# Kernel tuning notes

Hardware: AMD Instinct MI355X
Metric: run time of the kernel (lower is better)

The kernel has to match this reference:

```python
import jax, jax.numpy as jnp
import numpy as np

# scNET (vae_flag=False, cd=False, eval mode): genes x cells matrix;
# PPI graph over 3000 genes, KNN graph over 4096 cells.
N_GENES, N_CELLS = 3000, 4096          # col_dim, row_dim
INTER_R, EMBD_R = 512, 128             # gene (rows) encoder dims
INTER_C, EMBD_C = 1024, 256            # cell (cols) encoder dims
N_LAYERS = 2
KNN_E, PPI_E = 65536, 262144
SCALE_PARAM = 3.0                      # TransformerConvReducrLayer scale_param


def setup_inputs() -> dict:
    key = jax.random.key(0)
    ks = iter(jax.random.split(key, 64))
    def lin(shape):
        fan_in = shape[-2]
        return jax.random.normal(next(ks), shape, jnp.float32) / np.sqrt(fan_in)
    inp = {}
    inp["x"] = jax.random.normal(next(ks), (N_GENES, N_CELLS), jnp.float32)
    inp["knn_ei"] = jax.random.randint(next(ks), (2, KNN_E), 0, N_CELLS)
    inp["ppi_ei"] = jax.random.randint(next(ks), (2, PPI_E), 0, N_GENES)
    inp["rl_W"] = lin((N_CELLS, N_CELLS)); inp["rl_b"] = jnp.zeros((N_CELLS,), jnp.float32)
    inp["rs_Wl"] = lin((N_LAYERS, N_CELLS, N_CELLS)); inp["rs_Wr"] = lin((N_LAYERS, N_CELLS, N_CELLS))
    inp["rs_b"] = jnp.zeros((N_LAYERS, N_CELLS), jnp.float32)
    inp["cs_Wl"] = lin((N_LAYERS, N_GENES, N_GENES)); inp["cs_Wr"] = lin((N_LAYERS, N_GENES, N_GENES))
    inp["cs_b"] = jnp.zeros((N_LAYERS, N_GENES), jnp.float32)
    inp["rg_W"] = lin((N_CELLS, INTER_R)); inp["rg_b"] = jnp.zeros((INTER_R,), jnp.float32)
    for nm in ("rq", "rk", "rv", "rsk"):
        inp[nm + "_W"] = lin((INTER_R, EMBD_R)); inp[nm + "_b"] = jnp.zeros((EMBD_R,), jnp.float32)
    inp["cg_W"] = lin((N_GENES, INTER_C)); inp["cg_b"] = jnp.zeros((INTER_C,), jnp.float32)
    for nm in ("cq", "ck", "cv", "csk"):
        inp[nm + "_W"] = lin((INTER_C, EMBD_C)); inp[nm + "_b"] = jnp.zeros((EMBD_C,), jnp.float32)
    inp["d1_W"] = lin((EMBD_C, INTER_C)); inp["d1_b"] = jnp.zeros((INTER_C,), jnp.float32)
    inp["d2_W"] = lin((INTER_C, INTER_C)); inp["d2_b"] = jnp.zeros((INTER_C,), jnp.float32)
    inp["d3_W"] = lin((INTER_C, N_GENES)); inp["d3_b"] = jnp.zeros((N_GENES,), jnp.float32)
    return inp


def sage_conv(x, ei, Wl, Wr, b):
    # PyG SAGEConv (mean aggr, root weight): lin_l(mean_{j->i} x_j) + lin_r(x_i) + b
    n = x.shape[0]
    src, dst = ei[0], ei[1]
    s = jax.ops.segment_sum(x[src], dst, num_segments=n)
    cnt = jax.ops.segment_sum(jnp.ones((ei.shape[1],), x.dtype), dst, num_segments=n)
    agg = s / jnp.maximum(cnt, 1.0)[:, None]
    return agg @ Wl + x @ Wr + b


def gcn_conv(x, ei, W, b):
    # PyG GCNConv: self loops + symmetric D^-1/2 (A+I) D^-1/2 normalization
    n = x.shape[0]
    idx = jnp.arange(n)
    src = jnp.concatenate([ei[0], idx])
    dst = jnp.concatenate([ei[1], idx])
    deg = jax.ops.segment_sum(jnp.ones((src.shape[0],), x.dtype), dst, num_segments=n)
    dinv = jax.lax.rsqrt(jnp.maximum(deg, 1.0))
    h = x @ W
    msg = h[src] * (dinv[src] * dinv[dst])[:, None]
    return jax.ops.segment_sum(msg, dst, num_segments=n) + b


def transformer_conv(x, ei, Wq, bq, Wk, bk, Wv, bv, Ws, bs, scale_param):
    # PyG TransformerConv (heads=1). scale_param=None -> per-destination segment
    # softmax; otherwise scNET's globally sigmoid-normalized attention
    # (TransformerConvReducrLayer.message): global mean/std standardize -> sigmoid.
    n = x.shape[0]
    d = Wq.shape[1]
    src, dst = ei[0], ei[1]
    q = x @ Wq + bq
    k = x @ Wk + bk
    v = x @ Wv + bv
    alpha = (q[dst] * k[src]).sum(-1) / jnp.sqrt(jnp.asarray(d, x.dtype))  # [E]
    if scale_param is None:
        m = jax.ops.segment_max(alpha, dst, num_segments=n)
        e = jnp.exp(alpha - m[dst])
        z = jax.ops.segment_sum(e, dst, num_segments=n)
        alpha = e / (z[dst] + 1e-16)
    else:
        alpha = (alpha - alpha.mean()) / ((1.0 / scale_param) * jnp.std(alpha, ddof=1))
        alpha = jax.nn.sigmoid(alpha)
    out = jax.ops.segment_sum(v[src] * alpha[:, None], dst, num_segments=n)
    return out + (x @ Ws + bs)  # root skip (lin_skip)


def reference(x, knn_ei, ppi_ei, rl_W, rl_b, rs_Wl, rs_Wr, rs_b, cs_Wl, cs_Wr, cs_b,
              rg_W, rg_b, rq_W, rq_b, rk_W, rk_b, rv_W, rv_b, rsk_W, rsk_b,
              cg_W, cg_b, cq_W, cq_b, ck_W, ck_b, cv_W, cv_b, csk_W, csk_b,
              d1_W, d1_b, d2_W, d2_b, d3_W, d3_b):
    # MutaelEncoder: row linear then alternating col/row SAGE layers (dropout=id in eval)
    h = x @ rl_W + rl_b                                   # [G, C]
    for i in range(N_LAYERS):
        h = jax.nn.leaky_relu(sage_conv(h.T, knn_ei, cs_Wl[i], cs_Wr[i], cs_b[i]), 0.01).T
        h = jax.nn.leaky_relu(sage_conv(h, ppi_ei, rs_Wl[i], rs_Wr[i], rs_b[i]), 0.01)
    # rows (gene) DimEncoder: GCN -> LeakyReLU -> TransformerConv (softmax attention)
    r = jax.nn.leaky_relu(gcn_conv(h, ppi_ei, rg_W, rg_b), 0.01)
    row_embed = transformer_conv(r, ppi_ei, rq_W, rq_b, rk_W, rk_b, rv_W, rv_b, rsk_W, rsk_b, None)
    # cols (cell) DimEncoder (reducer): GCN -> LeakyReLU -> sigmoid-normalized attention
    c = jax.nn.leaky_relu(gcn_conv(h.T, knn_ei, cg_W, cg_b), 0.01)
    col_embed = transformer_conv(c, knn_ei, cq_W, cq_b, ck_W, ck_b, cv_W, cv_b, csk_W, csk_b, SCALE_PARAM)
    # FatureDecoder (cd=False): 3-layer MLP with ReLU (dropout=id in eval)
    d = jax.nn.relu(col_embed @ d1_W + d1_b)
    d = jax.nn.relu(d @ d2_W + d2_b)
    recon = d @ d3_W + d3_b                               # [C_cells, G]
    return row_embed, col_embed, recon
```

## Files before the change

### kernel.cpp

```cpp
#include <hip/hip_runtime.h>
#include <math.h>

#define N_GENES 3000
#define N_CELLS 4096
#define GPAD    3072
#define INTER_R 512
#define EMBD_R  128
#define INTER_C 1024
#define EMBD_C  256
#define KNN_E   65536
#define PPI_E   262144

typedef unsigned short u16;
typedef __bf16 bf16x8 __attribute__((ext_vector_type(8)));
typedef float f32x4 __attribute__((ext_vector_type(4)));

__device__ __forceinline__ float b2f(u16 u) {
  union { unsigned i; float f; } x; x.i = ((unsigned)u) << 16; return x.f;
}
__device__ __forceinline__ u16 f2b(float f) {
  union { float f; unsigned i; } x; x.f = f;
  unsigned r = (x.i + 0x7FFFu + ((x.i >> 16) & 1u)) >> 16;
  return (u16)r;
}

typedef const void __attribute__((address_space(1))) gvoid;
typedef void __attribute__((address_space(3))) svoid;
__device__ __forceinline__ void gload16(const void* g, void* l) {
  __builtin_amdgcn_global_load_lds((gvoid*)g, (svoid*)l, 16, 0, 0);
}

template <int OUTF32>
__global__ __launch_bounds__(256) void mgemm_k(
    const u16* __restrict__ A, int lda, const u16* __restrict__ BT, int ldb,
    const float* __restrict__ bias, void* __restrict__ Cv, int ldc,
    int M, int N, int K, int accum, int act, int nbx) {
  __shared__ u16 As[2][128 * 32];
  __shared__ u16 Bs[2][128 * 32];
  const int t = threadIdx.x;
  const int w = t >> 6, l = t & 63;
  const int wr = w >> 1, wc = w & 1;
  const int fr = l & 15, hi = l >> 4;

  int nwg = gridDim.x;
  int bid = blockIdx.x;
  int q = nwg >> 3, r = nwg & 7, xcd = bid & 7, seq = bid >> 3;
  int sid = (xcd < r ? xcd * (q + 1) : r * (q + 1) + (xcd - r) * q) + seq;
  int by = sid / nbx, bx = sid - by * nbx;
  const int row0 = by * 128, col0 = bx * 128;

  f32x4 acc[4][4];
#pragma unroll
  for (int i = 0; i < 4; i++)
#pragma unroll
    for (int j = 0; j < 4; j++) acc[i][j] = (f32x4){0.f, 0.f, 0.f, 0.f};

  const u16* Aad[2]; const u16* Bad[2];
  char* Alds[2]; char* Blds[2];
#pragma unroll
  for (int c = 0; c < 2; c++) {
    int P = (w * 2 + c) * 64 + l;
    int prow = P >> 2, pg = (P & 3) ^ (prow & 3);
    int ar = row0 + prow; ar = ar < M ? ar : M - 1;
    int br = col0 + prow; br = br < N ? br : N - 1;
    Aad[c] = A + (size_t)ar * lda + pg * 8;
    Bad[c] = BT + (size_t)br * ldb + pg * 8;
    Alds[c] = (char*)&As[0][0] + (w * 2 + c) * 1024;
    Blds[c] = (char*)&Bs[0][0] + (w * 2 + c) * 1024;
  }
  const int nt = K >> 5;
  auto stage = [&](int tt, int b) {
    int ko = tt << 5;
#pragma unroll
    for (int c = 0; c < 2; c++) {
      gload16(Aad[c] + ko, Alds[c] + b * 8192);
      gload16(Bad[c] + ko, Blds[c] + b * 8192);
    }
  };
  auto compute = [&](int tt) {
    const u16* Ab = As[tt & 1];
    const u16* Bb = Bs[tt & 1];
    bf16x8 af[4], bfr[4];
#pragma unroll
    for (int mi = 0; mi < 4; mi++) {
      int row = wr * 64 + mi * 16 + fr;
      af[mi] = *(const bf16x8*)&Ab[row * 32 + ((hi ^ (row & 3)) << 3)];
    }
#pragma unroll
    for (int ni = 0; ni < 4; ni++) {
      int row = wc * 64 + ni * 16 + fr;
      bfr[ni] = *(const bf16x8*)&Bb[row * 32 + ((hi ^ (row & 3)) << 3)];
    }
    __builtin_amdgcn_s_setprio(1);
#pragma unroll
    for (int mi = 0; mi < 4; mi++)
#pragma unroll
      for (int ni = 0; ni < 4; ni++)
        acc[mi][ni] = __builtin_amdgcn_mfma_f32_16x16x32_bf16(
            af[mi], bfr[ni], acc[mi][ni], 0, 0, 0);
    __builtin_amdgcn_s_setprio(0);
  };

  stage(0, 0);
  if (nt > 1) stage(1, 1);
  for (int tt = 0; tt < nt - 1; tt++) {
    asm volatile("s_waitcnt vmcnt(4)" ::: "memory");
    __builtin_amdgcn_sched_barrier(0);
    __builtin_amdgcn_s_barrier();
    __builtin_amdgcn_sched_barrier(0);
    compute(tt);
    __builtin_amdgcn_sched_barrier(0);
    __builtin_amdgcn_s_barrier();
    __builtin_amdgcn_sched_barrier(0);
    if (tt + 2 < nt) stage(tt + 2, tt & 1);
  }
  asm volatile("s_waitcnt vmcnt(0)" ::: "memory");
  __builtin_amdgcn_sched_barrier(0);
  __builtin_amdgcn_s_barrier();
  __builtin_amdgcn_sched_barrier(0);
  compute(nt - 1);

#pragma unroll
  for (int mi = 0; mi < 4; mi++) {
    int mb = row0 + wr * 64 + mi * 16 + hi * 4;
#pragma unroll
    for (int rr2 = 0; rr2 < 4; rr2++) {
      int m = mb + rr2;
      if (m >= M) continue;
#pragma unroll
      for (int ni = 0; ni < 4; ni++) {
        int n = col0 + wc * 64 + ni * 16 + fr;
        if (n >= N) continue;
        float v = acc[mi][ni][rr2];
        if (bias) v += bias[n];
        if (OUTF32) {
          float* C = (float*)Cv;
          if (accum) v += C[(size_t)m * ldc + n];
          if (act == 1) v = v > 0.f ? v : 0.01f * v;
          else if (act == 2) v = fmaxf(v, 0.f);
          C[(size_t)m * ldc + n] = v;
        } else {
          u16* C = (u16*)Cv;
          if (accum) v += b2f(C[(size_t)m * ldc + n]);
          if (act == 1) v = v > 0.f ? v : 0.01f * v;
          else if (act == 2) v = fmaxf(v, 0.f);
          C[(size_t)m * ldc + n] = f2b(v);
        }
      }
    }
  }
}

__global__ void cvtw_k(const float* __restrict__ in, int K, int Nw,
                       u16* __restrict__ out, int ldb, int Kpad) {
  __shared__ float tile[32][33];
  int k0 = blockIdx.y * 32, n0 = blockIdx.x * 32;
  int tx = threadIdx.x & 31, ty = threadIdx.x >> 5;
  for (int i = ty; i < 32; i += 8)
    tile[i][tx] = (k0 + i < K && n0 + tx < Nw) ? in[(size_t)(k0 + i) * Nw + n0 + tx] : 0.f;
  __syncthreads();
  for (int i = ty; i < 32; i += 8) {
    int n = n0 + i, k = k0 + tx;
    if (n < Nw && k < Kpad) out[(size_t)n * ldb + k] = f2b(tile[tx][i]);
  }
}

__global__ void tpad_k(const u16* __restrict__ in, int R, int C, int lin,
                       u16* __restrict__ out, int ldout) {
  __shared__ u16 tile[32][33];
  int r0 = blockIdx.y * 32, c0 = blockIdx.x * 32;
  int tx = threadIdx.x & 31, ty = threadIdx.x >> 5;
  for (int i = ty; i < 32; i += 8)
    tile[i][tx] = (r0 + i < R && c0 + tx < C) ? in[(size_t)(r0 + i) * lin + c0 + tx] : (u16)0;
  __syncthreads();
  for (int i = ty; i < 32; i += 8) {
    int c = c0 + i, r = r0 + tx;
    if (c < C && r < ldout) out[(size_t)c * ldout + r] = tile[tx][i];
  }
}

__global__ void cvtx_k(const float* __restrict__ in, u16* __restrict__ out, int n) {
  int i = (blockIdx.x * 256 + threadIdx.x) * 4;
  if (i >= n) return;
  float4 v = *(const float4*)&in[i];
  uint2 o;
  o.x = (unsigned)f2b(v.x) | ((unsigned)f2b(v.y) << 16);
  o.y = (unsigned)f2b(v.z) | ((unsigned)f2b(v.w) << 16);
  *(uint2*)&out[i] = o;
}

__global__ void catbias_k(const float* b0, const float* b1, const float* b2,
                          const float* b3, int seg, float* out) {
  int i = blockIdx.x * 256 + threadIdx.x;
  if (i >= 4 * seg) return;
  const float* s = i < seg ? b0 : i < 2 * seg ? b1 : i < 3 * seg ? b2 : b3;
  out[i] = s[i & (seg - 1)];
}

__global__ void zero_i32(int* __restrict__ p, int n) {
  int i = blockIdx.x * 256 + threadIdx.x;
  if (i < n) p[i] = 0;
}
__global__ void count_k(const int* __restrict__ dst, int E, int* __restrict__ cnt) {
  int e = blockIdx.x * 256 + threadIdx.x;
  if (e < E) atomicAdd(&cnt[dst[e]], 1);
}
__global__ __launch_bounds__(1024) void scan_k(const int* __restrict__ cnt,
                                               int* __restrict__ rs, int N) {
  __shared__ int sd[1024];
  int t = threadIdx.x;
  int per = (N + 1023) >> 10;
  int base = t * per;
  int loc[4];
  int s = 0;
  for (int u = 0; u < per; u++) {
    int idx = base + u;
    loc[u] = s;
    int v = (idx < N) ? cnt[idx] : 0;
    s += v;
  }
  sd[t] = s;
  __syncthreads();
  for (int off = 1; off < 1024; off <<= 1) {
    int v = (t >= off) ? sd[t - off] : 0;
    __syncthreads();
    sd[t] += v;
    __syncthreads();
  }
  int prev = (t > 0) ? sd[t - 1] : 0;
  for (int u = 0; u < per; u++) {
    int idx = base + u;
    if (idx < N) rs[idx] = prev + loc[u];
  }
  if (t == 0) rs[N] = sd[1023];
}
__global__ void fill_k(const int* __restrict__ src, const int* __restrict__ dst, int E,
                       const int* __restrict__ rs, int* cursor,
                       int* __restrict__ csrc, int* __restrict__ ceid) {
  int e = blockIdx.x * 256 + threadIdx.x;
  if (e >= E) return;
  int d = dst[e];
  int p = atomicAdd(&cursor[d], 1);
  int b = rs[d] + p;
  csrc[b] = src[e];
  ceid[b] = e;
}
__global__ void dinv_k(const int* __restrict__ rs, float* __restrict__ dinv, int N) {
  int i = blockIdx.x * 256 + threadIdx.x;
  if (i < N) dinv[i] = rsqrtf((float)(rs[i + 1] - rs[i] + 1));
}

__global__ void sage_agg_k(const u16* __restrict__ X, int ld, const int* __restrict__ rs,
                           const int* __restrict__ csrc, u16* __restrict__ out,
                           int D, int Dpad) {
  int i = blockIdx.y;
  int j8 = (blockIdx.x * 256 + threadIdx.x) * 8;
  if (j8 >= Dpad) return;
  uint4 zo = {0, 0, 0, 0};
  if (j8 >= D) { *(uint4*)&out[(size_t)i * ld + j8] = zo; return; }
  int s = rs[i], e = rs[i + 1];
  float a[8] = {0, 0, 0, 0, 0, 0, 0, 0};
  for (int p = s; p < e; p++) {
    uint4 v = *(const uint4*)&X[(size_t)csrc[p] * ld + j8];
    a[0] += b2f(v.x & 0xffff); a[1] += b2f(v.x >> 16);
    a[2] += b2f(v.y & 0xffff); a[3] += b2f(v.y >> 16);
    a[4] += b2f(v.z & 0xffff); a[5] += b2f(v.z >> 16);
    a[6] += b2f(v.w & 0xffff); a[7] += b2f(v.w >> 16);
  }
  float inv = 1.f / fmaxf((float)(e - s), 1.f);
  uint4 o;
  o.x = (unsigned)f2b(a[0] * inv) | ((unsigned)f2b(a[1] * inv) << 16);
  o.y = (unsigned)f2b(a[2] * inv) | ((unsigned)f2b(a[3] * inv) << 16);
  o.z = (unsigned)f2b(a[4] * inv) | ((unsigned)f2b(a[5] * inv) << 16);
  o.w = (unsigned)f2b(a[6] * inv) | ((unsigned)f2b(a[7] * inv) << 16);
  *(uint4*)&out[(size_t)i * ld + j8] = o;
}

__global__ void gcn_agg_k(const u16* __restrict__ HW, int ld, const int* __restrict__ rs,
                          const int* __restrict__ csrc, const float* __restrict__ dinv,
                          const float* __restrict__ bias, u16* __restrict__ out, int D) {
  int i = blockIdx.y;
  int j8 = (blockIdx.x * 256 + threadIdx.x) * 8;
  if (j8 >= D) return;
  int s = rs[i], e = rs[i + 1];
  float a[8] = {0, 0, 0, 0, 0, 0, 0, 0};
  for (int p = s; p < e; p++) {
    int sr = csrc[p];
    float w = dinv[sr];
    uint4 v = *(const uint4*)&HW[(size_t)sr * ld + j8];
    a[0] += b2f(v.x & 0xffff) * w; a[1] += b2f(v.x >> 16) * w;
    a[2] += b2f(v.y & 0xffff) * w; a[3] += b2f(v.y >> 16) * w;
    a[4] += b2f(v.z & 0xffff) * w; a[5] += b2f(v.z >> 16) * w;
    a[6] += b2f(v.w & 0xffff) * w; a[7] += b2f(v.w >> 16) * w;
  }
  float di = dinv[i];
  uint4 sv = *(const uint4*)&HW[(size_t)i * ld + j8];
  float sf[8] = {b2f(sv.x & 0xffff), b2f(sv.x >> 16), b2f(sv.y & 0xffff), b2f(sv.y >> 16),
                 b2f(sv.z & 0xffff), b2f(sv.z >> 16), b2f(sv.w & 0xffff), b2f(sv.w >> 16)};
  unsigned o[4];
#pragma unroll
  for (int q = 0; q < 4; q++) {
    float v0 = di * a[2 * q] + sf[2 * q] * di * di + bias[j8 + 2 * q];
    float v1 = di * a[2 * q + 1] + sf[2 * q + 1] * di * di + bias[j8 + 2 * q + 1];
    v0 = v0 > 0.f ? v0 : 0.01f * v0;
    v1 = v1 > 0.f ? v1 : 0.01f * v1;
    o[q] = (unsigned)f2b(v0) | ((unsigned)f2b(v1) << 16);
  }
  *(uint4*)&out[(size_t)i * ld + j8] = *(uint4*)o;
}

__global__ void attn_row_k(const u16* __restrict__ QKVS, const int* __restrict__ rs,
                           const int* __restrict__ csrc, float* __restrict__ out, int N) {
  int node = blockIdx.x * 4 + (threadIdx.x >> 6);
  if (node >= N) return;
  int lane = threadIdx.x & 63;
  const u16* base = QKVS + (size_t)node * 512;
  unsigned qb = *(const unsigned*)&base[lane * 2];
  float qx = b2f(qb & 0xffff), qy = b2f(qb >> 16);
  int s = rs[node], e = rs[node + 1];
  float m = -1e30f, z = 0.f, ax = 0.f, ay = 0.f;
  const float scale = 0.08838834764831845f;
  for (int p = s; p < e; p++) {
    const u16* kb = QKVS + (size_t)csrc[p] * 512;
    unsigned kw = *(const unsigned*)&kb[128 + lane * 2];
    float part = qx * b2f(kw & 0xffff) + qy * b2f(kw >> 16);
#pragma unroll
    for (int off = 32; off; off >>= 1) part += __shfl_xor(part, off);
    float a = part * scale;
    float mn = fmaxf(m, a);
    float sc = __expf(m - mn);
    float wv = __expf(a - mn);
    z = z * sc + wv;
    unsigned vw = *(const unsigned*)&kb[256 + lane * 2];
    ax = ax * sc + wv * b2f(vw & 0xffff);
    ay = ay * sc + wv * b2f(vw >> 16);
    m = mn;
  }
  float inv = (e == s) ? 0.f : 1.f / (z + 1e-16f);
  unsigned sw = *(const unsigned*)&base[384 + lane * 2];
  out[(size_t)node * 128 + lane * 2] = ax * inv + b2f(sw & 0xffff);
  out[(size_t)node * 128 + lane * 2 + 1] = ay * inv + b2f(sw >> 16);
}

__global__ void col_alpha_k(const u16* __restrict__ QKVS, const int* __restrict__ src,
                            const int* __restrict__ dst, float* __restrict__ alpha, int E) {
  int e = blockIdx.x * 4 + (threadIdx.x >> 6);
  if (e >= E) return;
  int lane = threadIdx.x & 63;
  uint2 qb = *(const uint2*)&QKVS[(size_t)dst[e] * 1024 + lane * 4];
  uint2 kb = *(const uint2*)&QKVS[(size_t)src[e] * 1024 + 256 + lane * 4];
  float p = b2f(qb.x & 0xffff) * b2f(kb.x & 0xffff) + b2f(qb.x >> 16) * b2f(kb.x >> 16) +
            b2f(qb.y & 0xffff) * b2f(kb.y & 0xffff) + b2f(qb.y >> 16) * b2f(kb.y >> 16);
#pragma unroll
  for (int off = 32; off; off >>= 1) p += __shfl_xor(p, off);
  if (lane == 0) alpha[e] = p * 0.0625f;
}

__global__ void stats_k(const float* __restrict__ alpha, int E, double* __restrict__ st) {
  __shared__ double s1[256], s2[256];
  int t = threadIdx.x;
  double a1 = 0, a2 = 0;
  for (int i = blockIdx.x * 256 + t; i < E; i += gridDim.x * 256) {
    double a = alpha[i];
    a1 += a; a2 += a * a;
  }
  s1[t] = a1; s2[t] = a2;
  __syncthreads();
  for (int off = 128; off; off >>= 1) {
    if (t < off) { s1[t] += s1[t + off]; s2[t] += s2[t + off]; }
    __syncthreads();
  }
  if (t == 0) { atomicAdd(&st[0], s1[0]); atomicAdd(&st[1], s2[0]); }
}

__global__ void col_attn_agg_k(const u16* __restrict__ QKVS, const float* __restrict__ alpha,
                               const int* __restrict__ rs, const int* __restrict__ csrc,
                               const int* __restrict__ ceid, const double* __restrict__ st,
                               float* __restrict__ outf, u16* __restrict__ outb, int E) {
  int i = blockIdx.x;
  int j = threadIdx.x;
  double mean = st[0] / E;
  double var = (st[1] - E * mean * mean) / (double)(E - 1);
  float rstd = (float)(1.0 / sqrt(var));
  float fm = (float)mean;
  int s = rs[i], e = rs[i + 1];
  float acc = 0.f;
  for (int p = s; p < e; p++) {
    float a = alpha[ceid[p]];
    float x = 3.0f * (a - fm) * rstd;
    float sg = 1.f / (1.f + __expf(-x));
    acc += sg * b2f(QKVS[(size_t)csrc[p] * 1024 + 512 + j]);
  }
  float res = acc + b2f(QKVS[(size_t)i * 1024 + 768 + j]);
  outf[(size_t)i * 256 + j] = res;
  outb[(size_t)i * 256 + j] = f2b(res);
}

extern "C" void kernel_launch(void* const* d_in, const int* in_sizes, int n_in,
                              void* d_out, int out_size, void* d_ws, size_t ws_size,
                              hipStream_t stream) {
  const float* x      = (const float*)d_in[0];
  const int*   knn_ei = (const int*)d_in[1];
  const int*   ppi_ei = (const int*)d_in[2];
  const float* rl_W   = (const float*)d_in[3];
  const float* rl_b   = (const float*)d_in[4];
  const float* rs_Wl  = (const float*)d_in[5];
  const float* rs_Wr  = (const float*)d_in[6];
  const float* rs_b   = (const float*)d_in[7];
  const float* cs_Wl  = (const float*)d_in[8];
  const float* cs_Wr  = (const float*)d_in[9];
  const float* cs_b   = (const float*)d_in[10];
  const float* rg_W   = (const float*)d_in[11];
  const float* rg_b   = (const float*)d_in[12];
  const float* rq_W   = (const float*)d_in[13];
  const float* rq_b   = (const float*)d_in[14];
  const float* rk_W   = (const float*)d_in[15];
  const float* rk_b   = (const float*)d_in[16];
  const float* rv_W   = (const float*)d_in[17];
  const float* rv_b   = (const float*)d_in[18];
  const float* rsk_W  = (const float*)d_in[19];
  const float* rsk_b  = (const float*)d_in[20];
  const float* cg_W   = (const float*)d_in[21];
  const float* cg_b   = (const float*)d_in[22];
  const float* cq_W   = (const float*)d_in[23];
  const float* cq_b   = (const float*)d_in[24];
  const float* ck_W   = (const float*)d_in[25];
  const float* ck_b   = (const float*)d_in[26];
  const float* cv_W   = (const float*)d_in[27];
  const float* cv_b   = (const float*)d_in[28];
  const float* csk_W  = (const float*)d_in[29];
  const float* csk_b  = (const float*)d_in[30];
  const float* d1_W   = (const float*)d_in[31];
  const float* d1_b   = (const float*)d_in[32];
  const float* d2_W   = (const float*)d_in[33];
  const float* d2_b   = (const float*)d_in[34];
  const float* d3_W   = (const float*)d_in[35];
  const float* d3_b   = (const float*)d_in[36];
  float* out = (float*)d_out;

  char* ws = (char*)d_ws;
  size_t off = 0;
  auto alloc = [&](size_t bytes) -> void* {
    void* p = ws + off;
    off = (off + bytes + 255) & ~(size_t)255;
    return p;
  };
  const size_t PB = (size_t)N_CELLS * GPAD * 2;
  u16* P0 = (u16*)alloc(PB);
  u16* P1 = (u16*)alloc(PB);
  u16* P2 = (u16*)alloc(PB);
  u16* P3 = (u16*)alloc(PB);
  u16* xb  = (u16*)alloc((size_t)N_GENES * N_CELLS * 2);
  u16* BTs = (u16*)alloc((size_t)N_CELLS * N_CELLS * 2);
  u16* CEb = (u16*)alloc((size_t)N_CELLS * EMBD_C * 2);
  float* catb = (float*)alloc(1024 * 4);
  int* knn_rs  = (int*)alloc((N_CELLS + 1) * 4);
  int* knn_cnt = (int*)alloc(N_CELLS * 4);
  int* knn_cur = (int*)alloc(N_CELLS * 4);
  int* knn_src = (int*)alloc(KNN_E * 4);
  int* knn_eid = (int*)alloc(KNN_E * 4);
  int* ppi_rs  = (int*)alloc((N_GENES + 1) * 4);
  int* ppi_cnt = (int*)alloc(N_GENES * 4);
  int* ppi_cur = (int*)alloc(N_GENES * 4);
  int* ppi_src = (int*)alloc(PPI_E * 4);
  int* ppi_eid = (int*)alloc(PPI_E * 4);
  float* dinv_knn = (float*)alloc(N_CELLS * 4);
  float* dinv_ppi = (float*)alloc(N_GENES * 4);
  float* alphaB   = (float*)alloc(KNN_E * 4);
  double* stats   = (double*)alloc(2 * 8);

  auto cvtw = [&](const float* W, int K, int Nw, u16* dst, int ldb, int Kpad) {
    dim3 g((Nw + 31) / 32, (Kpad + 31) / 32);
    cvtw_k<<<g, 256, 0, stream>>>(W, K, Nw, dst, ldb, Kpad);
  };
  auto mg = [&](const u16* A, int lda, const u16* BT, int ldb, const float* bias,
                void* C, int ldc, int M, int N, int K, int accum, int act, int outf32) {
    int nbx = (N + 127) / 128, nby = (M + 127) / 128;
    dim3 g(nbx * nby);
    if (outf32)
      mgemm_k<1><<<g, 256, 0, stream>>>(A, lda, BT, ldb, bias, C, ldc, M, N, K, accum, act, nbx);
    else
      mgemm_k<0><<<g, 256, 0, stream>>>(A, lda, BT, ldb, bias, C, ldc, M, N, K, accum, act, nbx);
  };
  auto tpad = [&](const u16* in, int R, int C, int lin, u16* o, int ldout) {
    dim3 g((C + 31) / 32, (ldout + 31) / 32);
    tpad_k<<<g, 256, 0, stream>>>(in, R, C, lin, o, ldout);
  };
  auto sage = [&](const u16* X, int ld, const int* rs, const int* csrc, u16* o,
                  int nodes, int D, int Dpad) {
    dim3 g((Dpad / 8 + 255) / 256, nodes);
    sage_agg_k<<<g, 256, 0, stream>>>(X, ld, rs, csrc, o, D, Dpad);
  };
  auto gcn = [&](const u16* HW, int ld, const int* rs, const int* csrc, const float* dinv,
                 const float* bias, u16* o, int nodes, int D) {
    dim3 g((D / 8 + 255) / 256, nodes);
    gcn_agg_k<<<g, 256, 0, stream>>>(HW, ld, rs, csrc, dinv, bias, o, D);
  };

  zero_i32<<<(N_CELLS + 255) / 256, 256, 0, stream>>>(knn_cnt, N_CELLS);
  count_k<<<(KNN_E + 255) / 256, 256, 0, stream>>>(knn_ei + KNN_E, KNN_E, knn_cnt);
  scan_k<<<1, 1024, 0, stream>>>(knn_cnt, knn_rs, N_CELLS);
  zero_i32<<<(N_CELLS + 255) / 256, 256, 0, stream>>>(knn_cur, N_CELLS);
  fill_k<<<(KNN_E + 255) / 256, 256, 0, stream>>>(knn_ei, knn_ei + KNN_E, KNN_E,
                                                  knn_rs, knn_cur, knn_src, knn_eid);
  dinv_k<<<(N_CELLS + 255) / 256, 256, 0, stream>>>(knn_rs, dinv_knn, N_CELLS);
  zero_i32<<<(N_GENES + 255) / 256, 256, 0, stream>>>(ppi_cnt, N_GENES);
  count_k<<<(PPI_E + 255) / 256, 256, 0, stream>>>(ppi_ei + PPI_E, PPI_E, ppi_cnt);
  scan_k<<<1, 1024, 0, stream>>>(ppi_cnt, ppi_rs, N_GENES);
  zero_i32<<<(N_GENES + 255) / 256, 256, 0, stream>>>(ppi_cur, N_GENES);
  fill_k<<<(PPI_E + 255) / 256, 256, 0, stream>>>(ppi_ei, ppi_ei + PPI_E, PPI_E,
                                                  ppi_rs, ppi_cur, ppi_src, ppi_eid);
  dinv_k<<<(N_GENES + 255) / 256, 256, 0, stream>>>(ppi_rs, dinv_ppi, N_GENES);

  cvtx_k<<<(N_GENES * N_CELLS / 4 + 255) / 256, 256, 0, stream>>>(
      x, xb, N_GENES * N_CELLS);
  cvtw(rl_W, N_CELLS, N_CELLS, BTs, N_CELLS, N_CELLS);
  mg(xb, N_CELLS, BTs, N_CELLS, rl_b, P0, N_CELLS, N_GENES, N_CELLS, N_CELLS, 0, 0, 0);

  for (int i = 0; i < 2; i++) {
    const float* cWl = cs_Wl + (size_t)i * N_GENES * N_GENES;
    const float* cWr = cs_Wr + (size_t)i * N_GENES * N_GENES;
    const float* cb  = cs_b + (size_t)i * N_GENES;
    const float* rWl = rs_Wl + (size_t)i * N_CELLS * N_CELLS;
    const float* rWr = rs_Wr + (size_t)i * N_CELLS * N_CELLS;
    const float* rb  = rs_b + (size_t)i * N_CELLS;
    tpad(P0, N_GENES, N_CELLS, N_CELLS, P1, GPAD);
    sage(P1, GPAD, knn_rs, knn_src, P2, N_CELLS, N_GENES, GPAD);
    cvtw(cWl, N_GENES, N_GENES, BTs, GPAD, GPAD);
    mg(P2, GPAD, BTs, GPAD, cb, P3, GPAD, N_CELLS, N_GENES, GPAD, 0, 0, 0);
    cvtw(cWr, N_GENES, N_GENES, BTs, GPAD, GPAD);
    mg(P1, GPAD, BTs, GPAD, nullptr, P3, GPAD, N_CELLS, N_GENES, GPAD, 1, 1, 0);
    tpad(P3, N_CELLS, N_GENES, GPAD, P2, N_CELLS);
    sage(P2, N_CELLS, ppi_rs, ppi_src, P1, N_GENES, N_CELLS, N_CELLS);
    cvtw(rWl, N_CELLS, N_CELLS, BTs, N_CELLS, N_CELLS);
    mg(P1, N_CELLS, BTs, N_CELLS, rb, P0, N_CELLS, N_GENES, N_CELLS, N_CELLS, 0, 0, 0);
    cvtw(rWr, N_CELLS, N_CELLS, BTs, N_CELLS, N_CELLS);
    mg(P2, N_CELLS, BTs, N_CELLS, nullptr, P0, N_CELLS, N_GENES, N_CELLS, N_CELLS, 1, 1, 0);
  }

  cvtw(rg_W, N_CELLS, INTER_R, BTs, N_CELLS, N_CELLS);
  mg(P0, N_CELLS, BTs, N_CELLS, nullptr, P1, INTER_R, N_GENES, INTER_R, N_CELLS, 0, 0, 0);
  gcn(P1, INTER_R, ppi_rs, ppi_src, dinv_ppi, rg_b, P2, N_GENES, INTER_R);
  cvtw(rq_W, INTER_R, EMBD_R, BTs + (size_t)0 * EMBD_R * INTER_R, INTER_R, INTER_R);
  cvtw(rk_W, INTER_R, EMBD_R, BTs + (size_t)1 * EMBD_R * INTER_R, INTER_R, INTER_R);
  cvtw(rv_W, INTER_R, EMBD_R, BTs + (size_t)2 * EMBD_R * INTER_R, INTER_R, INTER_R);
  cvtw(rsk_W, INTER_R, EMBD_R, BTs + (size_t)3 * EMBD_R * INTER_R, INTER_R, INTER_R);
  catbias_k<<<2, 256, 0, stream>>>(rq_b, rk_b, rv_b, rsk_b, EMBD_R, catb);
  mg(P2, INTER_R, BTs, INTER_R, catb, P1, 4 * EMBD_R, N_GENES, 4 * EMBD_R, INTER_R, 0, 0, 0);
  attn_row_k<<<(N_GENES + 3) / 4, 256, 0, stream>>>(P1, ppi_rs, ppi_src, out, N_GENES);

  tpad(P0, N_GENES, N_CELLS, N_CELLS, P1, GPAD);
  cvtw(cg_W, N_GENES, INTER_C, BTs, GPAD, GPAD);
  mg(P1, GPAD, BTs, GPAD, nullptr, P2, INTER_C, N_CELLS, INTER_C, GPAD, 0, 0, 0);
  gcn(P2, INTER_C, knn_rs, knn_src, dinv_knn, cg_b, P0, N_CELLS, INTER_C);
  cvtw(cq_W, INTER_C, EMBD_C, BTs + (size_t)0 * EMBD_C * INTER_C, INTER_C, INTER_C);
  cvtw(ck_W, INTER_C, EMBD_C, BTs + (size_t)1 * EMBD_C * INTER_C, INTER_C, INTER_C);
  cvtw(cv_W, INTER_C, EMBD_C, BTs + (size_t)2 * EMBD_C * INTER_C, INTER_C, INTER_C);
  cvtw(csk_W, INTER_C, EMBD_C, BTs + (size_t)3 * EMBD_C * INTER_C, INTER_C, INTER_C);
  catbias_k<<<4, 256, 0, stream>>>(cq_b, ck_b, cv_b, csk_b, EMBD_C, catb);
  mg(P0, INTER_C, BTs, INTER_C, catb, P1, 4 * EMBD_C, N_CELLS, 4 * EMBD_C, INTER_C, 0, 0, 0);
  col_alpha_k<<<KNN_E / 4, 256, 0, stream>>>(P1, knn_ei, knn_ei + KNN_E, alphaB, KNN_E);
  zero_i32<<<1, 256, 0, stream>>>((int*)stats, 4);
  stats_k<<<64, 256, 0, stream>>>(alphaB, KNN_E, stats);
  float* col_embed = out + (size_t)N_GENES * EMBD_R;
  col_attn_agg_k<<<N_CELLS, 256, 0, stream>>>(P1, alphaB, knn_rs, knn_src, knn_eid,
                                              stats, col_embed, CEb, KNN_E);

  float* recon = col_embed + (size_t)N_CELLS * EMBD_C;
  cvtw(d1_W, EMBD_C, INTER_C, BTs, EMBD_C, EMBD_C);
  mg(CEb, EMBD_C, BTs, EMBD_C, d1_b, P2, INTER_C, N_CELLS, INTER_C, EMBD_C, 0, 2, 0);
  cvtw(d2_W, INTER_C, INTER_C, BTs, INTER_C, INTER_C);
  mg(P2, INTER_C, BTs, INTER_C, d2_b, P3, INTER_C, N_CELLS, INTER_C, INTER_C, 0, 2, 0);
  cvtw(d3_W, INTER_C, N_GENES, BTs, INTER_C, INTER_C);
  mg(P3, INTER_C, BTs, INTER_C, d3_b, recon, N_GENES, N_CELLS, N_GENES, INTER_C, 0, 0, 1);
}
```

Baseline: 2.461 ms.

## Fuse SAGE lin_l and lin_r GEMMs via concatenated K and repack LDS tiles

Each SAGE layer's two GEMMs (aggregated features times Wl plus root features times Wr, with accumulate) become one GEMM with doubled K. The aggregated and root matrices sit side by side in one buffer, and the weights are concatenated along K. This removes a second pass that read and wrote the output and launched an extra kernel, and it drops the separate zero-padding writes. The GEMM's LDS layout also changes from 128x32 to 64x64 row pairs with a new swizzle, which could change bank conflicts. Buffers are re-aliased, which risks overlap mistakes.

```diff
diff --git a/kernel.cpp b/kernel.cpp
--- a/kernel.cpp
+++ b/kernel.cpp
@@ -35,15 +35,14 @@
     const u16* __restrict__ A, int lda, const u16* __restrict__ BT, int ldb,
     const float* __restrict__ bias, void* __restrict__ Cv, int ldc,
     int M, int N, int K, int accum, int act, int nbx) {
-  __shared__ u16 As[2][128 * 32];
-  __shared__ u16 Bs[2][128 * 32];
+  __shared__ u16 As[2][64 * 64];
+  __shared__ u16 Bs[2][64 * 64];
   const int t = threadIdx.x;
   const int w = t >> 6, l = t & 63;
   const int wr = w >> 1, wc = w & 1;
   const int fr = l & 15, hi = l >> 4;
 
-  int nwg = gridDim.x;
-  int bid = blockIdx.x;
+  int nwg = gridDim.x, bid = blockIdx.x;
   int q = nwg >> 3, r = nwg & 7, xcd = bid & 7, seq = bid >> 3;
   int sid = (xcd < r ? xcd * (q + 1) : r * (q + 1) + (xcd - r) * q) + seq;
   int by = sid / nbx, bx = sid - by * nbx;
@@ -60,13 +59,15 @@
 #pragma unroll
   for (int c = 0; c < 2; c++) {
     int P = (w * 2 + c) * 64 + l;
-    int prow = P >> 2, pg = (P & 3) ^ (prow & 3);
-    int ar = row0 + prow; ar = ar < M ? ar : M - 1;
-    int br = col0 + prow; br = br < N ? br : N - 1;
-    Aad[c] = A + (size_t)ar * lda + pg * 8;
-    Bad[c] = BT + (size_t)br * ldb + pg * 8;
-    Alds[c] = (char*)&As[0][0] + (w * 2 + c) * 1024;
-    Blds[c] = (char*)&Bs[0][0] + (w * 2 + c) * 1024;
+    int prow = P >> 3, s = P & 7;
+    int lr = prow * 2 + (s >> 2);
+    int g = (s & 3) ^ (prow & 3);
+    int ar = row0 + lr; ar = ar < M ? ar : M - 1;
+    int br = col0 + lr; br = br < N ? br : N - 1;
+    Aad[c] = A + (size_t)ar * lda + g * 8;
+    Bad[c] = BT + (size_t)br * ldb + g * 8;
+    Alds[c] = (char*)&As[0][0] + P * 16;
+    Blds[c] = (char*)&Bs[0][0] + P * 16;
   }
   const int nt = K >> 5;
   auto stage = [&](int tt, int b) {
@@ -84,12 +85,14 @@
 #pragma unroll
     for (int mi = 0; mi < 4; mi++) {
       int row = wr * 64 + mi * 16 + fr;
-      af[mi] = *(const bf16x8*)&Ab[row * 32 + ((hi ^ (row & 3)) << 3)];
+      int pr = row >> 1;
+      af[mi] = *(const bf16x8*)&Ab[pr * 64 + ((row & 1) * 4 + (hi ^ (pr & 3))) * 8];
     }
 #pragma unroll
     for (int ni = 0; ni < 4; ni++) {
       int row = wc * 64 + ni * 16 + fr;
-      bfr[ni] = *(const bf16x8*)&Bb[row * 32 + ((hi ^ (row & 3)) << 3)];
+      int pr = row >> 1;
+      bfr[ni] = *(const bf16x8*)&Bb[pr * 64 + ((row & 1) * 4 + (hi ^ (pr & 3))) * 8];
     }
     __builtin_amdgcn_s_setprio(1);
 #pragma unroll
@@ -166,7 +169,7 @@
 }
 
 __global__ void tpad_k(const u16* __restrict__ in, int R, int C, int lin,
-                       u16* __restrict__ out, int ldout) {
+                       u16* __restrict__ out, int ostride, int Rpad) {
   __shared__ u16 tile[32][33];
   int r0 = blockIdx.y * 32, c0 = blockIdx.x * 32;
   int tx = threadIdx.x & 31, ty = threadIdx.x >> 5;
@@ -175,7 +178,7 @@
   __syncthreads();
   for (int i = ty; i < 32; i += 8) {
     int c = c0 + i, r = r0 + tx;
-    if (c < C && r < ldout) out[(size_t)c * ldout + r] = tile[tx][i];
+    if (c < C && r < Rpad) out[(size_t)c * ostride + r] = tile[tx][i];
   }
 }
 
@@ -251,13 +254,10 @@
 }
 
 __global__ void sage_agg_k(const u16* __restrict__ X, int ld, const int* __restrict__ rs,
-                           const int* __restrict__ csrc, u16* __restrict__ out,
-                           int D, int Dpad) {
+                           const int* __restrict__ csrc, u16* __restrict__ out, int D) {
   int i = blockIdx.y;
   int j8 = (blockIdx.x * 256 + threadIdx.x) * 8;
-  if (j8 >= Dpad) return;
-  uint4 zo = {0, 0, 0, 0};
-  if (j8 >= D) { *(uint4*)&out[(size_t)i * ld + j8] = zo; return; }
+  if (j8 >= D) return;
   int s = rs[i], e = rs[i + 1];
   float a[8] = {0, 0, 0, 0, 0, 0, 0, 0};
   for (int p = s; p < e; p++) {
@@ -445,13 +445,11 @@
     off = (off + bytes + 255) & ~(size_t)255;
     return p;
   };
-  const size_t PB = (size_t)N_CELLS * GPAD * 2;
-  u16* P0 = (u16*)alloc(PB);
-  u16* P1 = (u16*)alloc(PB);
-  u16* P2 = (u16*)alloc(PB);
-  u16* P3 = (u16*)alloc(PB);
-  u16* xb  = (u16*)alloc((size_t)N_GENES * N_CELLS * 2);
-  u16* BTs = (u16*)alloc((size_t)N_CELLS * N_CELLS * 2);
+  u16* P0 = (u16*)alloc((size_t)N_GENES * N_CELLS * 2);
+  u16* P1 = (u16*)alloc((size_t)N_CELLS * GPAD * 2);
+  u16* P2 = (u16*)alloc((size_t)N_CELLS * GPAD * 2);
+  u16* CR = (u16*)alloc((size_t)N_CELLS * 2 * GPAD * 2);
+  u16* BTs = (u16*)alloc((size_t)N_CELLS * 2 * N_CELLS * 2);
   u16* CEb = (u16*)alloc((size_t)N_CELLS * EMBD_C * 2);
   float* catb = (float*)alloc(1024 * 4);
   int* knn_rs  = (int*)alloc((N_CELLS + 1) * 4);
@@ -468,6 +466,9 @@
   float* dinv_ppi = (float*)alloc(N_GENES * 4);
   float* alphaB   = (float*)alloc(KNN_E * 4);
   double* stats   = (double*)alloc(2 * 8);
+  u16* xb = CR;
+  u16* CA = CR;
+  u16* RA = CR;
 
   auto cvtw = [&](const float* W, int K, int Nw, u16* dst, int ldb, int Kpad) {
     dim3 g((Nw + 31) / 32, (Kpad + 31) / 32);
@@ -482,14 +483,14 @@
     else
       mgemm_k<0><<<g, 256, 0, stream>>>(A, lda, BT, ldb, bias, C, ldc, M, N, K, accum, act, nbx);
   };
-  auto tpad = [&](const u16* in, int R, int C, int lin, u16* o, int ldout) {
-    dim3 g((C + 31) / 32, (ldout + 31) / 32);
-    tpad_k<<<g, 256, 0, stream>>>(in, R, C, lin, o, ldout);
+  auto tpad = [&](const u16* in, int R, int C, int lin, u16* o, int ostride, int Rpad) {
+    dim3 g((C + 31) / 32, (Rpad + 31) / 32);
+    tpad_k<<<g, 256, 0, stream>>>(in, R, C, lin, o, ostride, Rpad);
   };
   auto sage = [&](const u16* X, int ld, const int* rs, const int* csrc, u16* o,
-                  int nodes, int D, int Dpad) {
-    dim3 g((Dpad / 8 + 255) / 256, nodes);
-    sage_agg_k<<<g, 256, 0, stream>>>(X, ld, rs, csrc, o, D, Dpad);
+                  int nodes, int D) {
+    dim3 g((D / 8 + 255) / 256, nodes);
+    sage_agg_k<<<g, 256, 0, stream>>>(X, ld, rs, csrc, o, D);
   };
   auto gcn = [&](const u16* HW, int ld, const int* rs, const int* csrc, const float* dinv,
                  const float* bias, u16* o, int nodes, int D) {
@@ -524,18 +525,17 @@
     const float* rWl = rs_Wl + (size_t)i * N_CELLS * N_CELLS;
     const float* rWr = rs_Wr + (size_t)i * N_CELLS * N_CELLS;
     const float* rb  = rs_b + (size_t)i * N_CELLS;
-    tpad(P0, N_GENES, N_CELLS, N_CELLS, P1, GPAD);
-    sage(P1, GPAD, knn_rs, knn_src, P2, N_CELLS, N_GENES, GPAD);
-    cvtw(cWl, N_GENES, N_GENES, BTs, GPAD, GPAD);
-    mg(P2, GPAD, BTs, GPAD, cb, P3, GPAD, N_CELLS, N_GENES, GPAD, 0, 0, 0);
-    cvtw(cWr, N_GENES, N_GENES, BTs, GPAD, GPAD);
-    mg(P1, GPAD, BTs, GPAD, nullptr, P3, GPAD, N_CELLS, N_GENES, GPAD, 1, 1, 0);
-    tpad(P3, N_CELLS, N_GENES, GPAD, P2, N_CELLS);
-    sage(P2, N_CELLS, ppi_rs, ppi_src, P1, N_GENES, N_CELLS, N_CELLS);
-    cvtw(rWl, N_CELLS, N_CELLS, BTs, N_CELLS, N_CELLS);
-    mg(P1, N_CELLS, BTs, N_CELLS, rb, P0, N_CELLS, N_GENES, N_CELLS, N_CELLS, 0, 0, 0);
-    cvtw(rWr, N_CELLS, N_CELLS, BTs, N_CELLS, N_CELLS);
-    mg(P2, N_CELLS, BTs, N_CELLS, nullptr, P0, N_CELLS, N_GENES, N_CELLS, N_CELLS, 1, 1, 0);
+    tpad(P0, N_GENES, N_CELLS, N_CELLS, CA + GPAD, 2 * GPAD, GPAD);
+    sage(CA + GPAD, 2 * GPAD, knn_rs, knn_src, CA, N_CELLS, GPAD);
+    cvtw(cWl, N_GENES, N_GENES, BTs, 2 * GPAD, GPAD);
+    cvtw(cWr, N_GENES, N_GENES, BTs + GPAD, 2 * GPAD, GPAD);
+    mg(CA, 2 * GPAD, BTs, 2 * GPAD, cb, P1, GPAD, N_CELLS, N_GENES, 2 * GPAD, 0, 1, 0);
+    tpad(P1, N_CELLS, N_GENES, GPAD, RA + N_CELLS, 2 * N_CELLS, N_CELLS);
+    sage(RA + N_CELLS, 2 * N_CELLS, ppi_rs, ppi_src, RA, N_GENES, N_CELLS);
+    cvtw(rWl, N_CELLS, N_CELLS, BTs, 2 * N_CELLS, N_CELLS);
+    cvtw(rWr, N_CELLS, N_CELLS, BTs + N_CELLS, 2 * N_CELLS, N_CELLS);
+    mg(RA, 2 * N_CELLS, BTs, 2 * N_CELLS, rb, P0, N_CELLS,
+       N_GENES, N_CELLS, 2 * N_CELLS, 0, 1, 0);
   }
 
   cvtw(rg_W, N_CELLS, INTER_R, BTs, N_CELLS, N_CELLS);
@@ -549,7 +549,7 @@
   mg(P2, INTER_R, BTs, INTER_R, catb, P1, 4 * EMBD_R, N_GENES, 4 * EMBD_R, INTER_R, 0, 0, 0);
   attn_row_k<<<(N_GENES + 3) / 4, 256, 0, stream>>>(P1, ppi_rs, ppi_src, out, N_GENES);
 
-  tpad(P0, N_GENES, N_CELLS, N_CELLS, P1, GPAD);
+  tpad(P0, N_GENES, N_CELLS, N_CELLS, P1, GPAD, GPAD);
   cvtw(cg_W, N_GENES, INTER_C, BTs, GPAD, GPAD);
   mg(P1, GPAD, BTs, GPAD, nullptr, P2, INTER_C, N_CELLS, INTER_C, GPAD, 0, 0, 0);
   gcn(P2, INTER_C, knn_rs, knn_src, dinv_knn, cg_b, P0, N_CELLS, INTER_C);
@@ -566,11 +566,13 @@
   col_attn_agg_k<<<N_CELLS, 256, 0, stream>>>(P1, alphaB, knn_rs, knn_src, knn_eid,
                                               stats, col_embed, CEb, KNN_E);
 
+  u16* D1 = CR;
+  u16* D2 = CR + (size_t)N_CELLS * INTER_C;
   float* recon = col_embed + (size_t)N_CELLS * EMBD_C;
   cvtw(d1_W, EMBD_C, INTER_C, BTs, EMBD_C, EMBD_C);
-  mg(CEb, EMBD_C, BTs, EMBD_C, d1_b, P2, INTER_C, N_CELLS, INTER_C, EMBD_C, 0, 2, 0);
+  mg(CEb, EMBD_C, BTs, EMBD_C, d1_b, D1, INTER_C, N_CELLS, INTER_C, EMBD_C, 0, 2, 0);
   cvtw(d2_W, INTER_C, INTER_C, BTs, INTER_C, INTER_C);
-  mg(P2, INTER_C, BTs, INTER_C, d2_b, P3, INTER_C, N_CELLS, INTER_C, INTER_C, 0, 2, 0);
+  mg(D1, INTER_C, BTs, INTER_C, d2_b, D2, INTER_C, N_CELLS, INTER_C, INTER_C, 0, 2, 0);
   cvtw(d3_W, INTER_C, N_GENES, BTs, INTER_C, INTER_C);
-  mg(P3, INTER_C, BTs, INTER_C, d3_b, recon, N_GENES, N_CELLS, N_GENES, INTER_C, 0, 0, 1);
-}
+  mg(D2, INTER_C, BTs, INTER_C, d3_b, recon, N_GENES, N_CELLS, N_GENES, INTER_C, 0, 0, 1);
+}
```

Result: no change. 2.434 ms (-1.1%).
